# Kernel optimization log

Measured on AMD Instinct MI355X. Metric: run time of the kernel, lower is better.

## Reference

```python
import jax, jax.numpy as jnp
import numpy as np

B, C, IMG, P = 64, 3, 224, 16
DIM, DEPTH, HEADS, HID, NCLS = 768, 12, 12, 3072, 1000
H_PATCH = IMG // P            # 14
NPATCH = H_PATCH * H_PATCH    # 196
PD = C * P * P                # 768 patch_dim
HD = DIM // HEADS             # 64
SCALE = HD ** -0.5


def layernorm(x, g, b, eps=1e-5):
    mu = jnp.mean(x, axis=-1, keepdims=True)
    var = jnp.mean((x - mu) ** 2, axis=-1, keepdims=True)
    return (x - mu) / jnp.sqrt(var + eps) * g + b


def setup_inputs() -> dict:
    key = jax.random.key(0)
    ks = iter(jax.random.split(key, 16))
    nrm = lambda shape, s=0.02: jax.random.normal(next(ks), shape, jnp.float32) * s
    return {
        "x": jax.random.normal(next(ks), (B, C, IMG, IMG), jnp.float32),
        "ln_p_g": jnp.ones((PD,), jnp.float32), "ln_p_b": jnp.zeros((PD,), jnp.float32),
        "W_patch": nrm((PD, DIM)), "b_patch": jnp.zeros((DIM,), jnp.float32),
        "ln_e_g": jnp.ones((DIM,), jnp.float32), "ln_e_b": jnp.zeros((DIM,), jnp.float32),
        "pos_emb": nrm((1, NPATCH + 1, DIM)),
        "cls_token": nrm((1, 1, DIM)),
        "ln_a_g": jnp.ones((DEPTH, DIM), jnp.float32), "ln_a_b": jnp.zeros((DEPTH, DIM), jnp.float32),
        "Wq": nrm((DEPTH, DIM, DIM)), "Wk": nrm((DEPTH, DIM, DIM)), "Wv": nrm((DEPTH, DIM, DIM)),
        "Wo": nrm((DEPTH, DIM, DIM)), "bo": jnp.zeros((DEPTH, DIM), jnp.float32),
        "ln_f_g": jnp.ones((DEPTH, DIM), jnp.float32), "ln_f_b": jnp.zeros((DEPTH, DIM), jnp.float32),
        "W1": nrm((DEPTH, DIM, HID)), "b1": jnp.zeros((DEPTH, HID), jnp.float32),
        "W2": nrm((DEPTH, HID, DIM)), "b2": jnp.zeros((DEPTH, DIM), jnp.float32),
        "ln_out_g": jnp.ones((DIM,), jnp.float32), "ln_out_b": jnp.zeros((DIM,), jnp.float32),
        "W_head": nrm((DIM, NCLS)), "b_head": jnp.zeros((NCLS,), jnp.float32),
    }


def reference(x, ln_p_g, ln_p_b, W_patch, b_patch, ln_e_g, ln_e_b, pos_emb, cls_token,
              ln_a_g, ln_a_b, Wq, Wk, Wv, Wo, bo, ln_f_g, ln_f_b, W1, b1, W2, b2,
              ln_out_g, ln_out_b, W_head, b_head):
    b = x.shape[0]
    # patch embed: 'b c (h h1) (w w1) -> b (h w) (h1 w1 c)'
    p = x.reshape(b, C, H_PATCH, P, H_PATCH, P)
    p = p.transpose(0, 2, 4, 3, 5, 1).reshape(b, NPATCH, PD)
    p = layernorm(p, ln_p_g, ln_p_b)
    p = p @ W_patch + b_patch
    p = layernorm(p, ln_e_g, ln_e_b)
    cls = jnp.broadcast_to(cls_token, (b, 1, DIM))
    z = jnp.concatenate([cls, p], axis=1) + pos_emb  # [b, 197, dim]
    n = z.shape[1]
    for i in range(DEPTH):
        # attention block (pre-LN inside Attention)
        xa = layernorm(z, ln_a_g[i], ln_a_b[i])
        q = (xa @ Wq[i]).reshape(b, n, HEADS, HD).transpose(0, 2, 1, 3)
        k = (xa @ Wk[i]).reshape(b, n, HEADS, HD).transpose(0, 2, 1, 3)
        v = (xa @ Wv[i]).reshape(b, n, HEADS, HD).transpose(0, 2, 1, 3)
        att = jax.nn.softmax(jnp.einsum('bhnd,bhmd->bhnm', q, k) * SCALE, axis=-1)
        o = jnp.einsum('bhnm,bhmd->bhnd', att, v).transpose(0, 2, 1, 3).reshape(b, n, DIM)
        z = z + (o @ Wo[i] + bo[i])
        # feed-forward block
        xf = layernorm(z, ln_f_g[i], ln_f_b[i])
        z = z + jax.nn.gelu(xf @ W1[i] + b1[i], approximate=False) @ W2[i] + b2[i]
    z = layernorm(z, ln_out_g, ln_out_b)
    logits = z[:, 0] @ W_head + b_head  # CLS token
    return jax.nn.softmax(logits, axis=1)
```

## Files before the change

kernel.cpp:

```cpp
#include <hip/hip_runtime.h>
#include <hip/hip_bf16.h>
#include <math.h>

#define NTOK 197

typedef __attribute__((ext_vector_type(8))) short bfx8;
typedef __attribute__((ext_vector_type(4))) float fx4;

#define GLOAD16(gsrc, ldst) __builtin_amdgcn_global_load_lds( \
    (const __attribute__((address_space(1))) void*)(gsrc),    \
    (__attribute__((address_space(3))) void*)(ldst), 16, 0, 0)

__device__ __forceinline__ float gelu_f(float x) {
    return 0.5f * x * (1.0f + erff(x * 0.70710678118654752f));
}

__global__ __launch_bounds__(256) void patch_ln_k(const float* __restrict__ x,
                                                  __hip_bfloat16* __restrict__ out,
                                                  const float* __restrict__ g,
                                                  const float* __restrict__ bt) {
    const int r = blockIdx.x;
    const int t = threadIdx.x;
    const int b = r / 196, p = r % 196;
    const int ph = p / 14, pw = p % 14;

    __shared__ float px[768];
    if (t < 192) {
        int rr = t >> 2, seg = t & 3;
        int c = rr >> 4, h1 = rr & 15;
        const float* src = x + (((size_t)b * 3 + c) * 224 + (ph * 16 + h1)) * 224
                             + pw * 16 + seg * 4;
        float4 v4 = *(const float4*)src;
        px[(h1 * 16 + seg * 4 + 0) * 3 + c] = v4.x;
        px[(h1 * 16 + seg * 4 + 1) * 3 + c] = v4.y;
        px[(h1 * 16 + seg * 4 + 2) * 3 + c] = v4.z;
        px[(h1 * 16 + seg * 4 + 3) * 3 + c] = v4.w;
    }
    __syncthreads();

    float v[3];
    #pragma unroll
    for (int i = 0; i < 3; ++i) v[i] = px[t + i * 256];
    float s = v[0] + v[1] + v[2];
    float sq = v[0]*v[0] + v[1]*v[1] + v[2]*v[2];
    #pragma unroll
    for (int off = 32; off; off >>= 1) { s += __shfl_xor(s, off); sq += __shfl_xor(sq, off); }
    __shared__ float ss[4], s2[4];
    const int w = t >> 6;
    if ((t & 63) == 0) { ss[w] = s; s2[w] = sq; }
    __syncthreads();
    s  = ss[0] + ss[1] + ss[2] + ss[3];
    sq = s2[0] + s2[1] + s2[2] + s2[3];
    const float inv = 1.0f / 768.0f;
    float mu = s * inv;
    float var = sq * inv - mu * mu;
    float rstd = rsqrtf(var + 1e-5f);
    __hip_bfloat16* o = out + (size_t)r * 768;
    #pragma unroll
    for (int i = 0; i < 3; ++i) {
        int d = t + i * 256;
        o[d] = (__hip_bfloat16)((v[i] - mu) * rstd * g[d] + bt[d]);
    }
}

template <typename OT>
__global__ __launch_bounds__(256) void ln_k(const float* __restrict__ in,
                                            OT* __restrict__ out,
                                            const float* __restrict__ g,
                                            const float* __restrict__ bt) {
    const int r = blockIdx.x;
    const int t = threadIdx.x;
    const float* xr = in + (size_t)r * 768;
    float v0 = xr[t], v1 = xr[t + 256], v2 = xr[t + 512];
    float s = v0 + v1 + v2;
    float sq = v0*v0 + v1*v1 + v2*v2;
    #pragma unroll
    for (int off = 32; off; off >>= 1) { s += __shfl_xor(s, off); sq += __shfl_xor(sq, off); }
    __shared__ float ss[4], s2[4];
    const int w = t >> 6;
    if ((t & 63) == 0) { ss[w] = s; s2[w] = sq; }
    __syncthreads();
    s  = ss[0] + ss[1] + ss[2] + ss[3];
    sq = s2[0] + s2[1] + s2[2] + s2[3];
    const float inv = 1.0f / 768.0f;
    float mu = s * inv;
    float var = sq * inv - mu * mu;
    float rstd = rsqrtf(var + 1e-5f);
    OT* o = out + (size_t)r * 768;
    o[t]       = (OT)((v0 - mu) * rstd * g[t]       + bt[t]);
    o[t + 256] = (OT)((v1 - mu) * rstd * g[t + 256] + bt[t + 256]);
    o[t + 512] = (OT)((v2 - mu) * rstd * g[t + 512] + bt[t + 512]);
}

__global__ __launch_bounds__(256) void ln_cls_k(const float* __restrict__ in,
                                                __hip_bfloat16* __restrict__ out,
                                                const float* __restrict__ g,
                                                const float* __restrict__ bt) {
    const int b = blockIdx.x;
    const int t = threadIdx.x;
    if (b >= 64) {
        #pragma unroll
        for (int i = 0; i < 3; ++i) out[(size_t)b * 768 + t + i * 256] = (__hip_bfloat16)0.0f;
        return;
    }
    const float* xr = in + (size_t)b * 197 * 768;
    float v0 = xr[t], v1 = xr[t + 256], v2 = xr[t + 512];
    float s = v0 + v1 + v2;
    float sq = v0*v0 + v1*v1 + v2*v2;
    #pragma unroll
    for (int off = 32; off; off >>= 1) { s += __shfl_xor(s, off); sq += __shfl_xor(sq, off); }
    __shared__ float ss[4], s2[4];
    const int w = t >> 6;
    if ((t & 63) == 0) { ss[w] = s; s2[w] = sq; }
    __syncthreads();
    s  = ss[0] + ss[1] + ss[2] + ss[3];
    sq = s2[0] + s2[1] + s2[2] + s2[3];
    const float inv = 1.0f / 768.0f;
    float mu = s * inv;
    float var = sq * inv - mu * mu;
    float rstd = rsqrtf(var + 1e-5f);
    __hip_bfloat16* o = out + (size_t)b * 768;
    o[t]       = (__hip_bfloat16)((v0 - mu) * rstd * g[t]       + bt[t]);
    o[t + 256] = (__hip_bfloat16)((v1 - mu) * rstd * g[t + 256] + bt[t + 256]);
    o[t + 512] = (__hip_bfloat16)((v2 - mu) * rstd * g[t + 512] + bt[t + 512]);
}

__global__ __launch_bounds__(256) void build_z_k(const float* __restrict__ pln,
                                                 const float* __restrict__ cls,
                                                 const float* __restrict__ pos,
                                                 float* __restrict__ z) {
    size_t idx = (size_t)blockIdx.x * 256 + threadIdx.x;
    int d  = idx % 768;
    size_t tkb = idx / 768;
    int tk = tkb % 197;
    int b  = tkb / 197;
    float v = (tk == 0) ? cls[d] : pln[((size_t)b * 196 + (tk - 1)) * 768 + d];
    z[idx] = v + pos[(size_t)tk * 768 + d];
}

__global__ __launch_bounds__(256) void wconv_k(const float* __restrict__ W,
                                               __hip_bfloat16* __restrict__ Wt,
                                               int K, int N, size_t ostride) {
    __shared__ float tl[64][65];
    const int t = threadIdx.x;
    const int n0 = blockIdx.x * 64, k0 = blockIdx.y * 64;
    const size_t ibase = (size_t)blockIdx.z * K * N;
    const size_t obase = (size_t)blockIdx.z * ostride;
    #pragma unroll
    for (int i = 0; i < 16; ++i) {
        int idx = i * 256 + t;
        int kl = idx >> 6, nl = idx & 63;
        tl[kl][nl] = W[ibase + (size_t)(k0 + kl) * N + n0 + nl];
    }
    __syncthreads();
    #pragma unroll
    for (int i = 0; i < 16; ++i) {
        int idx = i * 256 + t;
        int nl = idx >> 6, kl = idx & 63;
        Wt[obase + (size_t)(n0 + nl) * K + k0 + kl] = (__hip_bfloat16)tl[kl][nl];
    }
}

__global__ __launch_bounds__(256) void whT_k(const float* __restrict__ W,
                                             __hip_bfloat16* __restrict__ Wt) {
    __shared__ float tl[64][65];
    const int t = threadIdx.x;
    const int n0 = blockIdx.x * 64, k0 = blockIdx.y * 64;
    #pragma unroll
    for (int i = 0; i < 16; ++i) {
        int idx = i * 256 + t;
        int kl = idx >> 6, nl = idx & 63;
        int n = n0 + nl;
        tl[kl][nl] = (n < 1000) ? W[(size_t)(k0 + kl) * 1000 + n] : 0.f;
    }
    __syncthreads();
    #pragma unroll
    for (int i = 0; i < 16; ++i) {
        int idx = i * 256 + t;
        int nl = idx >> 6, kl = idx & 63;
        Wt[(size_t)(n0 + nl) * 768 + k0 + kl] = (__hip_bfloat16)tl[kl][nl];
    }
}

template <int EPI, typename OT>
__global__ __launch_bounds__(256) void mgemm_k(const __hip_bfloat16* __restrict__ A,
                                               const __hip_bfloat16* __restrict__ Wt,
                                               const float* __restrict__ bias,
                                               const float* __restrict__ resid,
                                               OT* __restrict__ C,
                                               int M, int N, int K) {
    __shared__ __align__(16) char sA[16384];
    __shared__ __align__(16) char sB[16384];
    const int t = threadIdx.x;
    const int lane = t & 63, w = t >> 6;
    const int wr = w >> 1, wc = w & 1;
    const int lrow = lane & 15, lgr = lane >> 4;
    const int bm = blockIdx.y * 128, bn = blockIdx.x * 128;

    const __hip_bfloat16* aSrc[4];
    const __hip_bfloat16* bSrc[4];
    #pragma unroll
    for (int i = 0; i < 4; ++i) {
        int q = t + i * 256;
        int r = q >> 3, c = q & 7;
        int gc = c ^ (r & 7);
        aSrc[i] = A  + (size_t)(bm + r) * K + gc * 8;
        bSrc[i] = Wt + (size_t)(bn + r) * K + gc * 8;
    }

    int aoff[4][2], boff[4][2];
    #pragma unroll
    for (int m = 0; m < 4; ++m) {
        int ra = wr * 64 + m * 16 + lrow;
        int rb = wc * 64 + m * 16 + lrow;
        #pragma unroll
        for (int ks = 0; ks < 2; ++ks) {
            aoff[m][ks] = ra * 128 + (((ks * 4 + lgr) ^ (ra & 7)) << 4);
            boff[m][ks] = rb * 128 + (((ks * 4 + lgr) ^ (rb & 7)) << 4);
        }
    }

    fx4 acc[4][4];
    #pragma unroll
    for (int m = 0; m < 4; ++m)
        #pragma unroll
        for (int n = 0; n < 4; ++n)
            #pragma unroll
            for (int e = 0; e < 4; ++e) acc[m][n][e] = 0.f;

    for (int k0 = 0; k0 < K; k0 += 64) {
        #pragma unroll
        for (int i = 0; i < 4; ++i) GLOAD16(aSrc[i] + k0, sA + (t + i * 256) * 16);
        #pragma unroll
        for (int i = 0; i < 4; ++i) GLOAD16(bSrc[i] + k0, sB + (t + i * 256) * 16);
        __syncthreads();
        #pragma unroll
        for (int ks = 0; ks < 2; ++ks) {
            bfx8 av[4], bv[4];
            #pragma unroll
            for (int m = 0; m < 4; ++m) {
                av[m] = *(const bfx8*)(sA + aoff[m][ks]);
                bv[m] = *(const bfx8*)(sB + boff[m][ks]);
            }
            #pragma unroll
            for (int m = 0; m < 4; ++m)
                #pragma unroll
                for (int n = 0; n < 4; ++n)
                    acc[m][n] = __builtin_amdgcn_mfma_f32_16x16x32_bf16(av[m], bv[n], acc[m][n], 0, 0, 0);
        }
        __syncthreads();
    }

    #pragma unroll
    for (int m = 0; m < 4; ++m) {
        #pragma unroll
        for (int n = 0; n < 4; ++n) {
            const int col = bn + wc * 64 + n * 16 + lrow;
            float bv2 = (EPI >= 1) ? bias[col] : 0.f;
            #pragma unroll
            for (int e = 0; e < 4; ++e) {
                const int row = bm + wr * 64 + m * 16 + lgr * 4 + e;
                if (row < M) {
                    float v = acc[m][n][e] + bv2;
                    if (EPI == 2) v = gelu_f(v);
                    if (EPI == 3) v += resid[(size_t)row * N + col];
                    C[(size_t)row * N + col] = (OT)v;
                }
            }
        }
    }
}

__global__ __launch_bounds__(256) void attn_k(const __hip_bfloat16* __restrict__ QKV,
                                              __hip_bfloat16* __restrict__ O) {
    __shared__ __align__(16) char Ks[224 * 128];
    __shared__ __align__(16) char VTs[64 * 464];
    __shared__ __align__(16) char Ps[4][7424];

    const int h = blockIdx.x;
    const int b = blockIdx.y;
    const int t = threadIdx.x;
    const int lane = t & 63, w = t >> 6;
    const int rho = lane & 15, g = lane >> 4;
    const size_t base = (size_t)b * NTOK * 2304;
    const int qoff = h * 64, koff = 768 + h * 64, voff = 1536 + h * 64;
    const size_t obase = ((size_t)b * NTOK) * 768 + h * 64;

    #pragma unroll
    for (int i = 0; i < 7; ++i) {
        int q = t + i * 256;
        int j = q >> 3, c = q & 7;
        int gc = c ^ (j & 7);
        GLOAD16(QKV + base + (size_t)j * 2304 + koff + gc * 8, Ks + q * 16);
    }
    #pragma unroll
    for (int i = 0; i < 7; ++i) {
        int q = t + i * 256;
        int tok = q >> 3, c = q & 7;
        bfx8 vv = {0, 0, 0, 0, 0, 0, 0, 0};
        if (tok < NTOK) vv = *(const bfx8*)(QKV + base + (size_t)tok * 2304 + voff + c * 8);
        #pragma unroll
        for (int u = 0; u < 8; ++u)
            *(unsigned short*)(VTs + (c * 8 + u) * 464 + tok * 2) = (unsigned short)vv[u];
    }
    __syncthreads();

    char* Pw = Ps[w];

    for (int qt = w; qt < 13; qt += 4) {
        const int q0 = qt * 16;
        fx4 s[13];
        #pragma unroll
        for (int nt = 0; nt < 13; ++nt)
            #pragma unroll
            for (int e = 0; e < 4; ++e) s[nt][e] = 0.f;
        #pragma unroll
        for (int ks = 0; ks < 2; ++ks) {
            bfx8 av = *(const bfx8*)(QKV + base + (size_t)(q0 + rho) * 2304 + qoff + ks * 32 + g * 8);
            #pragma unroll
            for (int nt = 0; nt < 13; ++nt) {
                int r = nt * 16 + rho;
                bfx8 bv = *(const bfx8*)(Ks + r * 128 + (((ks * 4 + g) ^ (r & 7)) << 4));
                s[nt] = __builtin_amdgcn_mfma_f32_16x16x32_bf16(av, bv, s[nt], 0, 0, 0);
            }
        }
        float mx[4] = {-1e30f, -1e30f, -1e30f, -1e30f};
        #pragma unroll
        for (int nt = 0; nt < 13; ++nt) {
            #pragma unroll
            for (int e = 0; e < 4; ++e) {
                float v = s[nt][e] * 0.125f;
                if (nt == 12 && rho >= 5) v = -1e30f;
                s[nt][e] = v;
                mx[e] = fmaxf(mx[e], v);
            }
        }
        #pragma unroll
        for (int off = 1; off < 16; off <<= 1)
            #pragma unroll
            for (int e = 0; e < 4; ++e) mx[e] = fmaxf(mx[e], __shfl_xor(mx[e], off));
        float sm[4] = {0.f, 0.f, 0.f, 0.f};
        #pragma unroll
        for (int nt = 0; nt < 13; ++nt)
            #pragma unroll
            for (int e = 0; e < 4; ++e) {
                float p = __expf(s[nt][e] - mx[e]);
                s[nt][e] = p;
                sm[e] += p;
            }
        #pragma unroll
        for (int off = 1; off < 16; off <<= 1)
            #pragma unroll
            for (int e = 0; e < 4; ++e) sm[e] += __shfl_xor(sm[e], off);
        float inv[4];
        #pragma unroll
        for (int e = 0; e < 4; ++e) inv[e] = 1.0f / sm[e];

        #pragma unroll
        for (int nt = 0; nt < 13; ++nt)
            #pragma unroll
            for (int e = 0; e < 4; ++e) {
                int row = g * 4 + e;
                int col = nt * 16 + rho;
                *(__hip_bfloat16*)(Pw + row * 464 + col * 2) =
                    (__hip_bfloat16)(s[nt][e] * inv[e]);
            }
        #pragma unroll
        for (int e = 0; e < 4; ++e)
            *(__hip_bfloat16*)(Pw + (g * 4 + e) * 464 + (208 + rho) * 2) = (__hip_bfloat16)0.0f;

        __builtin_amdgcn_sched_barrier(0);
        asm volatile("s_waitcnt lgkmcnt(0)" ::: "memory");
        __builtin_amdgcn_sched_barrier(0);

        #pragma unroll
        for (int dt = 0; dt < 4; ++dt) {
            fx4 o;
            #pragma unroll
            for (int e = 0; e < 4; ++e) o[e] = 0.f;
            #pragma unroll
            for (int ks = 0; ks < 7; ++ks) {
                bfx8 pa = *(const bfx8*)(Pw + rho * 464 + (ks * 4 + g) * 16);
                bfx8 bv = *(const bfx8*)(VTs + (dt * 16 + rho) * 464 + (ks * 4 + g) * 16);
                o = __builtin_amdgcn_mfma_f32_16x16x32_bf16(pa, bv, o, 0, 0, 0);
            }
            #pragma unroll
            for (int e = 0; e < 4; ++e) {
                int qrow = q0 + g * 4 + e;
                if (qrow < NTOK)
                    O[obase + (size_t)qrow * 768 + dt * 16 + rho] = (__hip_bfloat16)o[e];
            }
        }
    }
}

__global__ __launch_bounds__(256) void shead_k(const float* __restrict__ logits,
                                               const float* __restrict__ bh,
                                               float* __restrict__ out) {
    const int b = blockIdx.x;
    const int t = threadIdx.x;
    __shared__ float lg[1000];
    __shared__ float red[4];

    for (int c = t; c < 1000; c += 256) lg[c] = logits[(size_t)b * 1024 + c] + bh[c];
    __syncthreads();

    float m = -1e30f;
    for (int c = t; c < 1000; c += 256) m = fmaxf(m, lg[c]);
    #pragma unroll
    for (int off = 32; off; off >>= 1) m = fmaxf(m, __shfl_xor(m, off));
    if ((t & 63) == 0) red[t >> 6] = m;
    __syncthreads();
    m = fmaxf(fmaxf(red[0], red[1]), fmaxf(red[2], red[3]));
    __syncthreads();

    float sum = 0.f;
    for (int c = t; c < 1000; c += 256) sum += __expf(lg[c] - m);
    #pragma unroll
    for (int off = 32; off; off >>= 1) sum += __shfl_xor(sum, off);
    if ((t & 63) == 0) red[t >> 6] = sum;
    __syncthreads();
    sum = red[0] + red[1] + red[2] + red[3];
    const float invs = 1.0f / sum;
    for (int c = t; c < 1000; c += 256) out[(size_t)b * 1000 + c] = __expf(lg[c] - m) * invs;
}

extern "C" void kernel_launch(void* const* d_in, const int* in_sizes, int n_in,
                              void* d_out, int out_size, void* d_ws, size_t ws_size,
                              hipStream_t stream) {
    const float* x        = (const float*)d_in[0];
    const float* ln_p_g   = (const float*)d_in[1];
    const float* ln_p_b   = (const float*)d_in[2];
    const float* W_patch  = (const float*)d_in[3];
    const float* b_patch  = (const float*)d_in[4];
    const float* ln_e_g   = (const float*)d_in[5];
    const float* ln_e_b   = (const float*)d_in[6];
    const float* pos_emb  = (const float*)d_in[7];
    const float* cls_tok  = (const float*)d_in[8];
    const float* ln_a_g   = (const float*)d_in[9];
    const float* ln_a_b   = (const float*)d_in[10];
    const float* Wq       = (const float*)d_in[11];
    const float* Wk       = (const float*)d_in[12];
    const float* Wv       = (const float*)d_in[13];
    const float* Wo       = (const float*)d_in[14];
    const float* bo       = (const float*)d_in[15];
    const float* ln_f_g   = (const float*)d_in[16];
    const float* ln_f_b   = (const float*)d_in[17];
    const float* W1       = (const float*)d_in[18];
    const float* b1       = (const float*)d_in[19];
    const float* W2       = (const float*)d_in[20];
    const float* b2       = (const float*)d_in[21];
    const float* ln_out_g = (const float*)d_in[22];
    const float* ln_out_b = (const float*)d_in[23];
    const float* W_head   = (const float*)d_in[24];
    const float* b_head   = (const float*)d_in[25];

    typedef __hip_bfloat16 bf;
    const int M  = 12608;
    const int MP = 12672;
    char* p = (char*)d_ws;

    float* Z   = (float*)p;            p += (size_t)MP * 768 * 4;
    bf* XA     = (bf*)p;               p += (size_t)MP * 768 * 2;
    bf* QKV    = (bf*)p;               p += (size_t)MP * 2304 * 2;
    bf* OB     = (bf*)p;               p += (size_t)MP * 768 * 2;
    char* FFHc = p;                    p += (size_t)MP * 3072 * 2;
    bf* FFH    = (bf*)FFHc;
    float* PE  = (float*)FFHc;
    float* E2  = (float*)(FFHc + (size_t)MP * 768 * 4);
    bf* WQKVT  = (bf*)p;               p += (size_t)12 * 2304 * 768 * 2;
    bf* WoT    = (bf*)p;               p += (size_t)12 * 768 * 768 * 2;
    bf* W1T    = (bf*)p;               p += (size_t)12 * 3072 * 768 * 2;
    bf* W2T    = (bf*)p;               p += (size_t)12 * 768 * 3072 * 2;
    bf* WpT    = (bf*)p;               p += (size_t)768 * 768 * 2;
    bf* WhT    = (bf*)p;               p += (size_t)1024 * 768 * 2;
    bf* CLS    = (bf*)p;               p += (size_t)128 * 768 * 2;
    float* LOG = (float*)p;            p += (size_t)64 * 1024 * 4;

    const size_t QKVS = (size_t)2304 * 768;

    wconv_k<<<dim3(12, 12, 12), 256, 0, stream>>>(Wq, WQKVT,             768, 768,  QKVS);
    wconv_k<<<dim3(12, 12, 12), 256, 0, stream>>>(Wk, WQKVT + 768 * 768, 768, 768,  QKVS);
    wconv_k<<<dim3(12, 12, 12), 256, 0, stream>>>(Wv, WQKVT + 1536 * 768,768, 768,  QKVS);
    wconv_k<<<dim3(12, 12, 12), 256, 0, stream>>>(Wo, WoT,  768, 768,  (size_t)768 * 768);
    wconv_k<<<dim3(48, 12, 12), 256, 0, stream>>>(W1, W1T,  768, 3072, (size_t)3072 * 768);
    wconv_k<<<dim3(12, 48, 12), 256, 0, stream>>>(W2, W2T,  3072, 768, (size_t)768 * 3072);
    wconv_k<<<dim3(12, 12, 1),  256, 0, stream>>>(W_patch, WpT, 768, 768, 0);
    whT_k  <<<dim3(16, 12),     256, 0, stream>>>(W_head, WhT);

    patch_ln_k<<<12544, 256, 0, stream>>>(x, XA, ln_p_g, ln_p_b);
    mgemm_k<1, float><<<dim3(6, 98), 256, 0, stream>>>(XA, WpT, b_patch, nullptr, PE, 12544, 768, 768);
    ln_k<float><<<12544, 256, 0, stream>>>(PE, E2, ln_e_g, ln_e_b);
    build_z_k<<<37824, 256, 0, stream>>>(E2, cls_tok, pos_emb, Z);

    for (int i = 0; i < 12; ++i) {
        bf* WQKVT_i = WQKVT + (size_t)i * QKVS;
        bf* WoT_i   = WoT + (size_t)i * 768 * 768;
        bf* W1T_i   = W1T + (size_t)i * 3072 * 768;
        bf* W2T_i   = W2T + (size_t)i * 768 * 3072;

        ln_k<bf><<<M, 256, 0, stream>>>(Z, XA, ln_a_g + (size_t)i * 768, ln_a_b + (size_t)i * 768);
        mgemm_k<0, bf><<<dim3(18, 99), 256, 0, stream>>>(XA, WQKVT_i, nullptr, nullptr, QKV, M, 2304, 768);
        attn_k<<<dim3(12, 64), 256, 0, stream>>>(QKV, OB);
        mgemm_k<3, float><<<dim3(6, 99), 256, 0, stream>>>(OB, WoT_i, bo + (size_t)i * 768, Z, Z, M, 768, 768);
        ln_k<bf><<<M, 256, 0, stream>>>(Z, XA, ln_f_g + (size_t)i * 768, ln_f_b + (size_t)i * 768);
        mgemm_k<2, bf><<<dim3(24, 99), 256, 0, stream>>>(XA, W1T_i, b1 + (size_t)i * 3072, nullptr, FFH, M, 3072, 768);
        mgemm_k<3, float><<<dim3(6, 99), 256, 0, stream>>>(FFH, W2T_i, b2 + (size_t)i * 768, Z, Z, M, 768, 3072);
    }

    ln_cls_k<<<128, 256, 0, stream>>>(Z, CLS, ln_out_g, ln_out_b);
    mgemm_k<0, float><<<dim3(8, 1), 256, 0, stream>>>(CLS, WhT, nullptr, nullptr, LOG, 64, 1024, 768);
    shead_k<<<64, 256, 0, stream>>>(LOG, b_head, (float*)d_out);
}
```

Baseline: 5.038 ms.

## Add 256x256 double-buffered MFMA GEMM kernel and use it for all big GEMMs

Introduces a 512-thread GEMM kernel with 256x256 output tiles, an XOR-swizzled LDS layout, double buffering with global_load_lds, and 8x4 MFMA fragments per wave. All transformer and patch-embedding GEMMs switch to it. Row padding is raised to a multiple of 256 so the larger tiles never read past the buffers. The aim is more data reuse per LDS load and overlap of loads with compute. The cost is 128KB of LDS per block and far fewer blocks: only about 150 for the N=768 GEMMs, which can leave many CUs idle.

```diff
diff --git a/kernel.cpp b/kernel.cpp
--- a/kernel.cpp
+++ b/kernel.cpp
@@ -260,6 +260,127 @@
             #pragma unroll
             for (int e = 0; e < 4; ++e) {
                 const int row = bm + wr * 64 + m * 16 + lgr * 4 + e;
+                if (row < M) {
+                    float v = acc[m][n][e] + bv2;
+                    if (EPI == 2) v = gelu_f(v);
+                    if (EPI == 3) v += resid[(size_t)row * N + col];
+                    C[(size_t)row * N + col] = (OT)v;
+                }
+            }
+        }
+    }
+}
+
+template <int EPI, typename OT>
+__global__ __launch_bounds__(512, 2) void mgemm256_k(const __hip_bfloat16* __restrict__ A,
+                                                     const __hip_bfloat16* __restrict__ Wt,
+                                                     const float* __restrict__ bias,
+                                                     const float* __restrict__ resid,
+                                                     OT* __restrict__ C,
+                                                     int M, int N, int K) {
+    __shared__ __align__(16) char sA[2][32768];
+    __shared__ __align__(16) char sB[2][32768];
+    const int t = threadIdx.x;
+    const int lane = t & 63, w = t >> 6;
+    const int wr = w >> 2, wc = w & 3;
+    const int lrow = lane & 15, lgr = lane >> 4;
+    const int bm = blockIdx.y * 256, bn = blockIdx.x * 256;
+
+    const __hip_bfloat16* aSrc[4];
+    const __hip_bfloat16* bSrc[4];
+    #pragma unroll
+    for (int i = 0; i < 4; ++i) {
+        int q = t + i * 512;
+        int r = q >> 3, c = q & 7;
+        int gc = c ^ (r & 7);
+        aSrc[i] = A  + (size_t)(bm + r) * K + gc * 8;
+        bSrc[i] = Wt + (size_t)(bn + r) * K + gc * 8;
+    }
+
+    int aoff[8][2], boff[4][2];
+    #pragma unroll
+    for (int m = 0; m < 8; ++m) {
+        int ra = wr * 128 + m * 16 + lrow;
+        #pragma unroll
+        for (int ks = 0; ks < 2; ++ks)
+            aoff[m][ks] = ra * 128 + (((ks * 4 + lgr) ^ (ra & 7)) << 4);
+    }
+    #pragma unroll
+    for (int n = 0; n < 4; ++n) {
+        int rb = wc * 64 + n * 16 + lrow;
+        #pragma unroll
+        for (int ks = 0; ks < 2; ++ks)
+            boff[n][ks] = rb * 128 + (((ks * 4 + lgr) ^ (rb & 7)) << 4);
+    }
+
+    fx4 acc[8][4];
+    #pragma unroll
+    for (int m = 0; m < 8; ++m)
+        #pragma unroll
+        for (int n = 0; n < 4; ++n)
+            #pragma unroll
+            for (int e = 0; e < 4; ++e) acc[m][n][e] = 0.f;
+
+    const int NK = K >> 6;
+
+    #pragma unroll
+    for (int i = 0; i < 4; ++i) GLOAD16(aSrc[i], sA[0] + (t + i * 512) * 16);
+    #pragma unroll
+    for (int i = 0; i < 4; ++i) GLOAD16(bSrc[i], sB[0] + (t + i * 512) * 16);
+    __syncthreads();
+
+    int cur = 0;
+    for (int kt = 1; kt < NK; ++kt) {
+        const int nxt = cur ^ 1;
+        #pragma unroll
+        for (int i = 0; i < 4; ++i) GLOAD16(aSrc[i] + kt * 64, sA[nxt] + (t + i * 512) * 16);
+        #pragma unroll
+        for (int i = 0; i < 4; ++i) GLOAD16(bSrc[i] + kt * 64, sB[nxt] + (t + i * 512) * 16);
+        const char* bA = sA[cur];
+        const char* bB = sB[cur];
+        #pragma unroll
+        for (int ks = 0; ks < 2; ++ks) {
+            bfx8 av[8], bv[4];
+            #pragma unroll
+            for (int m = 0; m < 8; ++m) av[m] = *(const bfx8*)(bA + aoff[m][ks]);
+            #pragma unroll
+            for (int n = 0; n < 4; ++n) bv[n] = *(const bfx8*)(bB + boff[n][ks]);
+            #pragma unroll
+            for (int m = 0; m < 8; ++m)
+                #pragma unroll
+                for (int n = 0; n < 4; ++n)
+                    acc[m][n] = __builtin_amdgcn_mfma_f32_16x16x32_bf16(av[m], bv[n], acc[m][n], 0, 0, 0);
+        }
+        __syncthreads();
+        cur = nxt;
+    }
+    {
+        const char* bA = sA[cur];
+        const char* bB = sB[cur];
+        #pragma unroll
+        for (int ks = 0; ks < 2; ++ks) {
+            bfx8 av[8], bv[4];
+            #pragma unroll
+            for (int m = 0; m < 8; ++m) av[m] = *(const bfx8*)(bA + aoff[m][ks]);
+            #pragma unroll
+            for (int n = 0; n < 4; ++n) bv[n] = *(const bfx8*)(bB + boff[n][ks]);
+            #pragma unroll
+            for (int m = 0; m < 8; ++m)
+                #pragma unroll
+                for (int n = 0; n < 4; ++n)
+                    acc[m][n] = __builtin_amdgcn_mfma_f32_16x16x32_bf16(av[m], bv[n], acc[m][n], 0, 0, 0);
+        }
+    }
+
+    #pragma unroll
+    for (int m = 0; m < 8; ++m) {
+        #pragma unroll
+        for (int n = 0; n < 4; ++n) {
+            const int col = bn + wc * 64 + n * 16 + lrow;
+            float bv2 = (EPI >= 1) ? bias[col] : 0.f;
+            #pragma unroll
+            for (int e = 0; e < 4; ++e) {
+                const int row = bm + wr * 128 + m * 16 + lgr * 4 + e;
                 if (row < M) {
                     float v = acc[m][n][e] + bv2;
                     if (EPI == 2) v = gelu_f(v);
@@ -457,7 +578,7 @@
 
     typedef __hip_bfloat16 bf;
     const int M  = 12608;
-    const int MP = 12672;
+    const int MP = 12800;
     char* p = (char*)d_ws;
 
     float* Z   = (float*)p;            p += (size_t)MP * 768 * 4;
@@ -489,7 +610,7 @@
     whT_k  <<<dim3(16, 12),     256, 0, stream>>>(W_head, WhT);
 
     patch_ln_k<<<12544, 256, 0, stream>>>(x, XA, ln_p_g, ln_p_b);
-    mgemm_k<1, float><<<dim3(6, 98), 256, 0, stream>>>(XA, WpT, b_patch, nullptr, PE, 12544, 768, 768);
+    mgemm256_k<1, float><<<dim3(3, 49), 512, 0, stream>>>(XA, WpT, b_patch, nullptr, PE, 12544, 768, 768);
     ln_k<float><<<12544, 256, 0, stream>>>(PE, E2, ln_e_g, ln_e_b);
     build_z_k<<<37824, 256, 0, stream>>>(E2, cls_tok, pos_emb, Z);
 
@@ -500,12 +621,12 @@
         bf* W2T_i   = W2T + (size_t)i * 768 * 3072;
 
         ln_k<bf><<<M, 256, 0, stream>>>(Z, XA, ln_a_g + (size_t)i * 768, ln_a_b + (size_t)i * 768);
-        mgemm_k<0, bf><<<dim3(18, 99), 256, 0, stream>>>(XA, WQKVT_i, nullptr, nullptr, QKV, M, 2304, 768);
+        mgemm256_k<0, bf><<<dim3(9, 50), 512, 0, stream>>>(XA, WQKVT_i, nullptr, nullptr, QKV, M, 2304, 768);
         attn_k<<<dim3(12, 64), 256, 0, stream>>>(QKV, OB);
-        mgemm_k<3, float><<<dim3(6, 99), 256, 0, stream>>>(OB, WoT_i, bo + (size_t)i * 768, Z, Z, M, 768, 768);
+        mgemm256_k<3, float><<<dim3(3, 50), 512, 0, stream>>>(OB, WoT_i, bo + (size_t)i * 768, Z, Z, M, 768, 768);
         ln_k<bf><<<M, 256, 0, stream>>>(Z, XA, ln_f_g + (size_t)i * 768, ln_f_b + (size_t)i * 768);
-        mgemm_k<2, bf><<<dim3(24, 99), 256, 0, stream>>>(XA, W1T_i, b1 + (size_t)i * 3072, nullptr, FFH, M, 3072, 768);
-        mgemm_k<3, float><<<dim3(6, 99), 256, 0, stream>>>(FFH, W2T_i, b2 + (size_t)i * 768, Z, Z, M, 768, 3072);
+        mgemm256_k<2, bf><<<dim3(12, 50), 512, 0, stream>>>(XA, W1T_i, b1 + (size_t)i * 3072, nullptr, FFH, M, 3072, 768);
+        mgemm256_k<3, float><<<dim3(3, 50), 512, 0, stream>>>(FFH, W2T_i, b2 + (size_t)i * 768, Z, Z, M, 768, 3072);
     }
 
     ln_cls_k<<<128, 256, 0, stream>>>(Z, CLS, ln_out_g, ln_out_b);
```

Measured after the change: 6.480 ms. 1.29x slower.
